# Kernel tuning notes

Measured on AMD Instinct MI355X. Metric: run time of the kernel, lower is better.

The kernel has to match this reference:

```python
import jax, jax.numpy as jnp
import numpy as np

B_, H_, W_, C_ = 8, 56, 56, 96
D_ = int(C_ * 2.0)          # d_inner = 192
N_ = 16                     # d_state
K_ = 4                      # scan directions
R_ = (C_ + 15) // 16        # dt_rank 'auto' = 6
MLP_H = 4 * C_
EPS = 1e-5


def setup_inputs() -> dict:
    key = jax.random.key(0)
    ks = jax.random.split(key, 16)
    s = 0.02
    rn = lambda k, sh, sc=1.0: jax.random.normal(k, sh, dtype=jnp.float32) * sc
    return dict(
        x=rn(ks[0], (B_, H_, W_, C_)),
        ln1_w=jnp.ones((C_,), jnp.float32), ln1_b=jnp.zeros((C_,), jnp.float32),
        in_proj_w=rn(ks[1], (2 * D_, C_), s),
        conv_w=rn(ks[2], (D_, 1, 3, 3), s), conv_b=jnp.zeros((D_,), jnp.float32),
        x_proj_w=rn(ks[3], (K_, R_ + 2 * N_, D_), s),
        dt_proj_w=rn(ks[4], (K_, D_, R_), s),
        dt_proj_b=rn(ks[5], (K_, D_), 0.1),
        A_logs=jax.random.uniform(ks[6], (K_ * D_, N_), jnp.float32, 0.0, 3.0),
        Ds=jnp.ones((K_ * D_,), jnp.float32),
        out_norm_w=jnp.ones((D_,), jnp.float32), out_norm_b=jnp.zeros((D_,), jnp.float32),
        out_proj_w=rn(ks[7], (C_, D_), s),
        ln2_w=jnp.ones((C_,), jnp.float32), ln2_b=jnp.zeros((C_,), jnp.float32),
        fc1_w=rn(ks[8], (MLP_H, C_), s), fc1_b=jnp.zeros((MLP_H,), jnp.float32),
        fc2_w=rn(ks[9], (C_, MLP_H), s), fc2_b=jnp.zeros((C_,), jnp.float32),
    )


def layer_norm(x, w, b):
    m = x.mean(-1, keepdims=True)
    v = ((x - m) ** 2).mean(-1, keepdims=True)
    return (x - m) / jnp.sqrt(v + EPS) * w + b


def ss2d(x, in_proj_w, conv_w, conv_b, x_proj_w, dt_proj_w, dt_proj_b,
         A_logs, Ds, out_norm_w, out_norm_b, out_proj_w):
    Bn, Hh, Ww, C = x.shape
    L = Hh * Ww
    xz = x @ in_proj_w.T                       # (B,H,W,2D)
    xc, z = jnp.split(xz, 2, axis=-1)
    xc = xc.transpose(0, 3, 1, 2)              # (B,D,H,W)
    xc = jax.lax.conv_general_dilated(xc, conv_w, (1, 1), 'SAME',
                                      feature_group_count=D_)
    xc = jax.nn.silu(xc + conv_b[None, :, None, None])
    # cross-scan: 4 traversal orders, each (B,D,L)
    x0 = xc.reshape(Bn, D_, L)
    x1 = xc.transpose(0, 1, 3, 2).reshape(Bn, D_, L)
    xs = jnp.stack([x0, x1, x0[..., ::-1], x1[..., ::-1]], axis=1)  # (B,K,D,L)
    xdbl = jnp.einsum('bkdl,kcd->bkcl', xs, x_proj_w)
    dts, Bs, Cs = jnp.split(xdbl, [R_, R_ + N_], axis=2)            # (B,K,R,L),(B,K,N,L)x2
    dts = jnp.einsum('bkrl,kdr->bkdl', dts, dt_proj_w)
    dts = jax.nn.softplus(dts + dt_proj_b[None, :, :, None])        # (B,K,D,L)
    A = -jnp.exp(A_logs).reshape(K_, D_, N_)                        # (K,D,N)

    def step(h, inp):
        xt, dtt, Bt, Ct = inp                  # (B,K,D),(B,K,D),(B,K,N),(B,K,N)
        h = h * jnp.exp(dtt[..., None] * A) + (dtt * xt)[..., None] * Bt[:, :, None, :]
        return h, jnp.einsum('bkdn,bkn->bkd', h, Ct)

    inps = (xs.transpose(3, 0, 1, 2), dts.transpose(3, 0, 1, 2),
            Bs.transpose(3, 0, 1, 2), Cs.transpose(3, 0, 1, 2))
    h0 = jnp.zeros((Bn, K_, D_, N_), jnp.float32)
    _, ys = jax.lax.scan(step, h0, inps)       # (L,B,K,D)
    ys = ys.transpose(1, 2, 3, 0)              # (B,K,D,L)
    ys = ys + Ds.reshape(K_, D_)[None, :, :, None] * xs
    # cross-merge: undo flips and transposed order
    y = ys[:, 0] + ys[:, 2, :, ::-1]
    y = y + (ys[:, 1] + ys[:, 3, :, ::-1]).reshape(Bn, D_, Ww, Hh) \
            .transpose(0, 1, 3, 2).reshape(Bn, D_, L)
    y = y.transpose(0, 2, 1).reshape(Bn, Hh, Ww, D_)
    y = layer_norm(y, out_norm_w, out_norm_b)
    y = y * jax.nn.silu(z)
    return y @ out_proj_w.T


def reference(x, ln1_w, ln1_b, in_proj_w, conv_w, conv_b, x_proj_w, dt_proj_w,
              dt_proj_b, A_logs, Ds, out_norm_w, out_norm_b, out_proj_w,
              ln2_w, ln2_b, fc1_w, fc1_b, fc2_w, fc2_b):
    # norm -> SS2D -> residual
    x = x + ss2d(layer_norm(x, ln1_w, ln1_b), in_proj_w, conv_w, conv_b,
                 x_proj_w, dt_proj_w, dt_proj_b, A_logs, Ds,
                 out_norm_w, out_norm_b, out_proj_w)
    # norm -> MLP -> residual
    h = layer_norm(x, ln2_w, ln2_b)
    h = jax.nn.gelu(h @ fc1_w.T + fc1_b) @ fc2_w.T + fc2_b
    return x + h
```

## Files before the change

kernel.cpp:

```cpp
#include <hip/hip_runtime.h>
#include <hip/hip_bf16.h>

typedef __hip_bfloat16 bf16;
typedef short bf16x8 __attribute__((ext_vector_type(8)));
typedef float f32x4 __attribute__((ext_vector_type(4)));

#define BBATCH 8
#define HHH 56
#define WWW 56
#define CCH 96
#define DIN 192
#define NST 16
#define KDIR 4
#define RDT 6
#define LLEN 3136
#define BLTOT 25088
#define SSEG 64
#define SEGL 49
#define PJC 38
#define PJW 152
#define PJS 40
#define PJS1 24
#define MLPH 384

#if defined(__has_builtin)
#if __has_builtin(__builtin_amdgcn_exp2f)
#define EXP2F(x) __builtin_amdgcn_exp2f(x)
#endif
#if __has_builtin(__builtin_amdgcn_logf)
#define LOG2F_(x) __builtin_amdgcn_logf(x)
#endif
#endif
#ifndef EXP2F
#define EXP2F(x) __expf((x) * 0.69314718056f)
#endif
#ifndef LOG2F_
#define LOG2F_(x) (__logf(x) * 1.44269504f)
#endif
#define LOG2E 1.44269504f

__device__ __forceinline__ float b2f(bf16 v) { return __bfloat162float(v); }
__device__ __forceinline__ bf16  f2b(float v) { return __float2bfloat16(v); }
__device__ __forceinline__ unsigned short f2bu(float f) {
    union { bf16 h; unsigned short u; } c; c.h = __float2bfloat16(f); return c.u;
}
__device__ __forceinline__ float sigm(float x) { return 1.f / (1.f + __expf(-x)); }
__device__ __forceinline__ float softplusf(float x) {
    float t = EXP2F(-fabsf(x) * LOG2E);
    return fmaxf(x, 0.f) + 0.69314718f * LOG2F_(1.f + t);
}
__device__ __forceinline__ float geluf(float v) {
    float u = 0.7978845608028654f * (v + 0.044715f * v * v * v);
    float ey = __expf(2.f * u);
    float th = 1.f - 2.f / (ey + 1.f);
    return 0.5f * v * (1.f + th);
}

__device__ __forceinline__ int pos_map(int k, int l) {
    if (k & 2) l = LLEN - 1 - l;
    if (k & 1) { int q = l / WWW; int r = l - q * WWW; return r * WWW + q; }
    return l;
}

__global__ __launch_bounds__(256) void ln_rows(
    const float* __restrict__ xin, const float* __restrict__ w,
    const float* __restrict__ b, unsigned short* __restrict__ xn) {
    int row = blockIdx.x * 4 + (threadIdx.x >> 6);
    int lane = threadIdx.x & 63;
    const float* xr = xin + (size_t)row * 96;
    float2 v = make_float2(0.f, 0.f);
    if (lane < 48) v = *(const float2*)&xr[lane * 2];
    float s = v.x + v.y, s2 = v.x * v.x + v.y * v.y;
    for (int o = 32; o; o >>= 1) {
        s += __shfl_down(s, o);
        s2 += __shfl_down(s2, o);
    }
    s = __shfl(s, 0); s2 = __shfl(s2, 0);
    float m = s * (1.f / 96.f);
    float var = s2 * (1.f / 96.f) - m * m;
    float rs = rsqrtf(var + 1e-5f);
    if (lane < 48) {
        float o0 = (v.x - m) * rs * w[lane * 2] + b[lane * 2];
        float o1 = (v.y - m) * rs * w[lane * 2 + 1] + b[lane * 2 + 1];
        ushort2 u; u.x = f2bu(o0); u.y = f2bu(o1);
        *(ushort2*)&xn[(size_t)row * 96 + lane * 2] = u;
    }
}

template<int N, int K, int EPI>
__global__ __launch_bounds__(256) void gemm_mfma(
    const unsigned short* __restrict__ X, const float* __restrict__ W,
    const float* __restrict__ bias, const float* __restrict__ res,
    void* __restrict__ out0v, void* __restrict__ out1v) {
    __shared__ unsigned short a_sh[256 * 40];
    __shared__ unsigned short b_sh[64 * 40];
    const int t = threadIdx.x;
    const int P0 = blockIdx.x * 256;
    const int N0 = blockIdx.y * 64;
    const int w = t >> 6, lane = t & 63, q = lane >> 4, nl = lane & 15;
    f32x4 acc[4][4];
#pragma unroll
    for (int i = 0; i < 4; ++i)
#pragma unroll
        for (int j = 0; j < 4; ++j)
            acc[i][j] = (f32x4){0.f, 0.f, 0.f, 0.f};
    for (int k0 = 0; k0 < K; k0 += 32) {
        __syncthreads();
#pragma unroll
        for (int it = 0; it < 4; ++it) {
            int idx = t + it * 256;
            int pr = idx >> 2, kq = idx & 3;
            uint4 v = *(const uint4*)&X[(size_t)(P0 + pr) * K + k0 + kq * 8];
            *(uint4*)&a_sh[pr * 40 + kq * 8] = v;
        }
#pragma unroll
        for (int it = 0; it < 2; ++it) {
            int idx = t + it * 256;
            int nr = idx >> 3, kq = idx & 7;
            int ng = N0 + nr; if (ng > N - 1) ng = N - 1;
            float4 v = *(const float4*)&W[(size_t)ng * K + k0 + kq * 4];
            ushort4 u;
            u.x = f2bu(v.x); u.y = f2bu(v.y); u.z = f2bu(v.z); u.w = f2bu(v.w);
            *(ushort4*)&b_sh[nr * 40 + kq * 4] = u;
        }
        __syncthreads();
        bf16x8 af[4], bfr[4];
#pragma unroll
        for (int mf = 0; mf < 4; ++mf)
            af[mf] = *(const bf16x8*)&a_sh[(w * 64 + mf * 16 + nl) * 40 + q * 8];
#pragma unroll
        for (int nf = 0; nf < 4; ++nf)
            bfr[nf] = *(const bf16x8*)&b_sh[(nf * 16 + nl) * 40 + q * 8];
#pragma unroll
        for (int mf = 0; mf < 4; ++mf)
#pragma unroll
            for (int nf = 0; nf < 4; ++nf)
                acc[mf][nf] = __builtin_amdgcn_mfma_f32_16x16x32_bf16(
                    af[mf], bfr[nf], acc[mf][nf], 0, 0, 0);
    }
#pragma unroll
    for (int mf = 0; mf < 4; ++mf) {
#pragma unroll
        for (int nf = 0; nf < 4; ++nf) {
#pragma unroll
            for (int r = 0; r < 4; ++r) {
                float v = acc[mf][nf][r];
                size_t pos = (size_t)P0 + w * 64 + mf * 16 + q * 4 + r;
                int n = N0 + nf * 16 + nl;
                if constexpr (EPI == 0) {
                    unsigned short* xc = (unsigned short*)out0v;
                    unsigned short* zz = (unsigned short*)out1v;
                    if (n < 192) xc[pos * 192 + n] = f2bu(v);
                    else         zz[pos * 192 + (n - 192)] = f2bu(v);
                } else if constexpr (EPI == 1) {
                    if (n < 152) ((float*)out0v)[pos * 152 + n] = v;
                } else if constexpr (EPI == 2) {
                    if (n < 96) ((float*)out0v)[pos * 96 + n] = res[pos * 96 + n] + v;
                } else if constexpr (EPI == 3) {
                    ((unsigned short*)out0v)[pos * 384 + n] = f2bu(geluf(v + bias[n]));
                } else {
                    if (n < 96) ((float*)out0v)[pos * 96 + n] =
                        res[pos * 96 + n] + bias[n] + v;
                }
            }
        }
    }
}

__global__ __launch_bounds__(256) void k2_conv(
    const unsigned short* __restrict__ xcpre, const float* __restrict__ cw,
    const float* __restrict__ cb, unsigned short* __restrict__ xconv) {
    int idx = blockIdx.x * 256 + threadIdx.x;
    int dd = idx % 96;
    int P = idx / 96;
    int d0 = dd * 2;
    int b = P / LLEN, l = P - b * LLEN;
    int h = l / WWW, w = l - h * WWW;
    float acc0 = cb[d0], acc1 = cb[d0 + 1];
#pragma unroll
    for (int i = 0; i < 3; ++i) {
        int hh = h + i - 1;
        if (hh < 0 || hh >= HHH) continue;
#pragma unroll
        for (int j = 0; j < 3; ++j) {
            int ww = w + j - 1;
            if (ww < 0 || ww >= WWW) continue;
            ushort2 xv = *(const ushort2*)&xcpre[
                ((size_t)(b * LLEN + hh * WWW + ww)) * DIN + d0];
            union { unsigned short u; bf16 h_; } c0, c1;
            c0.u = xv.x; c1.u = xv.y;
            acc0 = fmaf(b2f(c0.h_), cw[d0 * 9 + i * 3 + j], acc0);
            acc1 = fmaf(b2f(c1.h_), cw[(d0 + 1) * 9 + i * 3 + j], acc1);
        }
    }
    acc0 = acc0 * sigm(acc0);
    acc1 = acc1 * sigm(acc1);
    ushort2 o; o.x = f2bu(acc0); o.y = f2bu(acc1);
    *(ushort2*)&xconv[(size_t)P * DIN + d0] = o;
}

__global__ __launch_bounds__(192) void k4_scan1(
    const bf16* __restrict__ xconv, const float* __restrict__ proj,
    const float* __restrict__ dtw, const float* __restrict__ dtb,
    const float* __restrict__ Alog, float* __restrict__ hloc,
    float* __restrict__ tsum) {
    __shared__ float pl[SEGL * PJS1];
    __shared__ int posl[SEGL];
    const int bid = blockIdx.x;
    const int s = bid & 63, k = (bid >> 6) & 3, b = bid >> 8;
    const int d = threadIdx.x;
    const int l0 = s * SEGL;
    for (int q = d; q < SEGL * 22; q += 192) {
        int st = q / 22, c = q - st * 22;
        int p = pos_map(k, l0 + st);
        int ofs = (c < 6) ? c : c + 2;
        pl[st * PJS1 + ofs] = proj[(size_t)(b * LLEN + p) * PJW + k * PJC + c];
    }
    if (d < SEGL) posl[d] = pos_map(k, l0 + d) * DIN;
    float w6[RDT];
#pragma unroll
    for (int r = 0; r < RDT; ++r) w6[r] = dtw[(k * DIN + d) * RDT + r];
    const float bias = dtb[k * DIN + d];
    float a2[NST];
#pragma unroll
    for (int n = 0; n < NST; ++n)
        a2[n] = -__expf(Alog[(k * DIN + d) * NST + n]) * LOG2E;
    float h[NST];
#pragma unroll
    for (int n = 0; n < NST; ++n) h[n] = 0.f;
    float T = 0.f;
    __syncthreads();
    const bf16* xg = xconv + (size_t)b * LLEN * DIN + d;
    for (int bt = 0; bt < 7; ++bt) {
        int off7[7]; float xv7[7];
#pragma unroll
        for (int i = 0; i < 7; ++i) off7[i] = posl[bt * 7 + i];
#pragma unroll
        for (int i = 0; i < 7; ++i) xv7[i] = b2f(xg[off7[i]]);
#pragma unroll
        for (int i = 0; i < 7; ++i) {
            const float* rowf = &pl[(bt * 7 + i) * PJS1];
            float4 g0 = *(const float4*)(rowf);
            float2 g1 = *(const float2*)(rowf + 4);
            float dtv = bias;
            dtv = fmaf(g0.x, w6[0], dtv); dtv = fmaf(g0.y, w6[1], dtv);
            dtv = fmaf(g0.z, w6[2], dtv); dtv = fmaf(g0.w, w6[3], dtv);
            dtv = fmaf(g1.x, w6[4], dtv); dtv = fmaf(g1.y, w6[5], dtv);
            dtv = softplusf(dtv);
            T += dtv;
            float u = dtv * xv7[i];
#pragma unroll
            for (int g = 0; g < 4; ++g) {
                float4 Bv = *(const float4*)(rowf + 8 + 4 * g);
                float e0 = EXP2F(dtv * a2[4 * g + 0]);
                float e1 = EXP2F(dtv * a2[4 * g + 1]);
                float e2 = EXP2F(dtv * a2[4 * g + 2]);
                float e3 = EXP2F(dtv * a2[4 * g + 3]);
                h[4 * g + 0] = fmaf(h[4 * g + 0], e0, u * Bv.x);
                h[4 * g + 1] = fmaf(h[4 * g + 1], e1, u * Bv.y);
                h[4 * g + 2] = fmaf(h[4 * g + 2], e2, u * Bv.z);
                h[4 * g + 3] = fmaf(h[4 * g + 3], e3, u * Bv.w);
            }
        }
    }
    size_t base = ((size_t)bid * DIN + d) * NST;
#pragma unroll
    for (int n = 0; n < NST; ++n) hloc[base + n] = h[n];
    tsum[bid * DIN + d] = T;
}

__global__ __launch_bounds__(256) void k5_carry(
    const float* hloc, const float* __restrict__ tsum,
    const float* __restrict__ Alog, float* hin) {
    int g = blockIdx.x * 256 + threadIdx.x;
    int n = g & 15;
    int dk = g >> 4;
    int d = dk % DIN;
    int bk = dk / DIN;
    int k = bk & 3;
    float a2 = -__expf(Alog[(k * DIN + d) * NST + n]) * LOG2E;
    float Hc = 0.f;
    for (int s = 0; s < SSEG; ++s) {
        int bid = bk * SSEG + s;
        size_t idx = ((size_t)bid * DIN + d) * NST + n;
        float hl = hloc[idx];
        float Tv = tsum[bid * DIN + d];
        hin[idx] = Hc;
        Hc = fmaf(EXP2F(a2 * Tv), Hc, hl);
    }
}

__global__ __launch_bounds__(192) void k6_scan2(
    const bf16* __restrict__ xconv, const float* __restrict__ proj,
    const float* __restrict__ dtw, const float* __restrict__ dtb,
    const float* __restrict__ Alog, const float* __restrict__ Dsp,
    const float* __restrict__ hin, bf16* __restrict__ ysm) {
    __shared__ float pl[SEGL * PJS];
    __shared__ int posl[SEGL];
    const int bid = blockIdx.x;
    const int s = bid & 63, k = (bid >> 6) & 3, b = bid >> 8;
    const int d = threadIdx.x;
    const int l0 = s * SEGL;
    for (int q = d; q < SEGL * PJC; q += 192) {
        int st = q / PJC, c = q - st * PJC;
        int p = pos_map(k, l0 + st);
        int ofs = (c < 6) ? c : c + 2;
        pl[st * PJS + ofs] = proj[(size_t)(b * LLEN + p) * PJW + k * PJC + c];
    }
    if (d < SEGL) posl[d] = pos_map(k, l0 + d) * DIN;
    float w6[RDT];
#pragma unroll
    for (int r = 0; r < RDT; ++r) w6[r] = dtw[(k * DIN + d) * RDT + r];
    const float bias = dtb[k * DIN + d];
    const float dsv = Dsp[k * DIN + d];
    float a2[NST];
#pragma unroll
    for (int n = 0; n < NST; ++n)
        a2[n] = -__expf(Alog[(k * DIN + d) * NST + n]) * LOG2E;
    float h[NST];
    size_t hbase = ((size_t)bid * DIN + d) * NST;
#pragma unroll
    for (int n = 0; n < NST; ++n) h[n] = hin[hbase + n];
    __syncthreads();
    const bf16* xg = xconv + (size_t)b * LLEN * DIN + d;
    bf16* ysg = ysm + ((size_t)(b * KDIR + k) * LLEN) * DIN + d;
    for (int bt = 0; bt < 7; ++bt) {
        int off7[7]; float xv7[7];
#pragma unroll
        for (int i = 0; i < 7; ++i) off7[i] = posl[bt * 7 + i];
#pragma unroll
        for (int i = 0; i < 7; ++i) xv7[i] = b2f(xg[off7[i]]);
#pragma unroll
        for (int i = 0; i < 7; ++i) {
            const float* rowf = &pl[(bt * 7 + i) * PJS];
            float4 g0 = *(const float4*)(rowf);
            float2 g1 = *(const float2*)(rowf + 4);
            float dtv = bias;
            dtv = fmaf(g0.x, w6[0], dtv); dtv = fmaf(g0.y, w6[1], dtv);
            dtv = fmaf(g0.z, w6[2], dtv); dtv = fmaf(g0.w, w6[3], dtv);
            dtv = fmaf(g1.x, w6[4], dtv); dtv = fmaf(g1.y, w6[5], dtv);
            dtv = softplusf(dtv);
            float u = dtv * xv7[i];
            float y = dsv * xv7[i];
#pragma unroll
            for (int g = 0; g < 4; ++g) {
                float4 Bv = *(const float4*)(rowf + 8 + 4 * g);
                float4 Cv = *(const float4*)(rowf + 24 + 4 * g);
                float e0 = EXP2F(dtv * a2[4 * g + 0]);
                float e1 = EXP2F(dtv * a2[4 * g + 1]);
                float e2 = EXP2F(dtv * a2[4 * g + 2]);
                float e3 = EXP2F(dtv * a2[4 * g + 3]);
                h[4 * g + 0] = fmaf(h[4 * g + 0], e0, u * Bv.x);
                h[4 * g + 1] = fmaf(h[4 * g + 1], e1, u * Bv.y);
                h[4 * g + 2] = fmaf(h[4 * g + 2], e2, u * Bv.z);
                h[4 * g + 3] = fmaf(h[4 * g + 3], e3, u * Bv.w);
                y = fmaf(h[4 * g + 0], Cv.x, y);
                y = fmaf(h[4 * g + 1], Cv.y, y);
                y = fmaf(h[4 * g + 2], Cv.z, y);
                y = fmaf(h[4 * g + 3], Cv.w, y);
            }
            ysg[off7[i]] = f2b(y);
        }
    }
}

__global__ __launch_bounds__(256) void k65_merge(
    const bf16* __restrict__ ysm, const bf16* __restrict__ z,
    const float* __restrict__ onw, const float* __restrict__ onb,
    bf16* __restrict__ ymod) {
    __shared__ float rb[16 * DIN];
    __shared__ float ps[256], pq[256];
    __shared__ float mrow[16], srow[16];
    const int t = threadIdx.x;
    const int P0 = blockIdx.x * 16;
    for (int q = t; q < 16 * DIN; q += 256) {
        int pos = q / DIN, c = q - pos * DIN;
        int P = P0 + pos;
        int b = P / LLEN, l = P - b * LLEN;
        size_t base = ((size_t)(b * KDIR) * LLEN + l) * DIN + c;
        size_t pstr = (size_t)LLEN * DIN;
        float v = b2f(ysm[base]) + b2f(ysm[base + pstr]) +
                  b2f(ysm[base + 2 * pstr]) + b2f(ysm[base + 3 * pstr]);
        rb[q] = v;
    }
    __syncthreads();
    {
        int pos = t >> 4, part = t & 15;
        float s = 0.f, s2 = 0.f;
        for (int i = 0; i < 12; ++i) {
            float v = rb[pos * DIN + part * 12 + i];
            s += v; s2 += v * v;
        }
        ps[pos * 16 + part] = s; pq[pos * 16 + part] = s2;
    }
    __syncthreads();
    if (t < 16) {
        float s = 0.f, s2 = 0.f;
        for (int i = 0; i < 16; ++i) { s += ps[t * 16 + i]; s2 += pq[t * 16 + i]; }
        float m = s * (1.f / DIN);
        float v = s2 * (1.f / DIN) - m * m;
        mrow[t] = m; srow[t] = rsqrtf(v + 1e-5f);
    }
    __syncthreads();
    for (int q = t; q < 16 * DIN; q += 256) {
        int pos = q / DIN, c = q - pos * DIN;
        int P = P0 + pos;
        float v = (rb[q] - mrow[pos]) * srow[pos] * onw[c] + onb[c];
        float zv = b2f(z[(size_t)P * DIN + c]);
        v *= zv * sigm(zv);
        ymod[(size_t)P * DIN + c] = f2b(v);
    }
}

extern "C" void kernel_launch(void* const* d_in, const int* in_sizes, int n_in,
                              void* d_out, int out_size, void* d_ws, size_t ws_size,
                              hipStream_t stream) {
    const float* x      = (const float*)d_in[0];
    const float* ln1w   = (const float*)d_in[1];
    const float* ln1b   = (const float*)d_in[2];
    const float* inpW   = (const float*)d_in[3];
    const float* convW  = (const float*)d_in[4];
    const float* convB  = (const float*)d_in[5];
    const float* xprojW = (const float*)d_in[6];
    const float* dtW    = (const float*)d_in[7];
    const float* dtB    = (const float*)d_in[8];
    const float* Alog   = (const float*)d_in[9];
    const float* Dsp    = (const float*)d_in[10];
    const float* onw    = (const float*)d_in[11];
    const float* onb    = (const float*)d_in[12];
    const float* outW   = (const float*)d_in[13];
    const float* ln2w   = (const float*)d_in[14];
    const float* ln2b   = (const float*)d_in[15];
    const float* fc1W   = (const float*)d_in[16];
    const float* fc1b   = (const float*)d_in[17];
    const float* fc2W   = (const float*)d_in[18];
    const float* fc2b   = (const float*)d_in[19];
    float* out = (float*)d_out;

    char* ws = (char*)d_ws;
    unsigned short* z_us    = (unsigned short*)(ws + 0);
    bf16*  z_bf             = (bf16*)z_us;
    bf16*  xconv_bf         = (bf16*)(ws + 9633792);
    float* proj_f           = (float*)(ws + 19267584);
    bf16*  ymod_bf          = (bf16*)(ws + 19267584);
    unsigned short* xn_us   = (unsigned short*)(ws + 34521088);
    float* tsum_f           = (float*)(ws + 34521088);
    unsigned short* xcpre_us= (unsigned short*)(ws + 39337984);
    float* hloc_f           = (float*)(ws + 48971776);
    float* hin_f            = hloc_f;
    float* y1_f             = (float*)(ws + 48971776);
    unsigned short* y1n_us  = (unsigned short*)(ws + 58605568);
    bf16*  ysm_bf           = (bf16*)(ws + 74137600);
    unsigned short* hmlp_us = (unsigned short*)(ws + 74137600);

    ln_rows<<<6272, 256, 0, stream>>>(x, ln1w, ln1b, xn_us);
    gemm_mfma<384, 96, 0><<<dim3(98, 6), 256, 0, stream>>>(
        xn_us, inpW, nullptr, nullptr, xcpre_us, z_us);
    k2_conv<<<9408, 256, 0, stream>>>(xcpre_us, convW, convB,
                                      (unsigned short*)xconv_bf);
    gemm_mfma<152, 192, 1><<<dim3(98, 3), 256, 0, stream>>>(
        (const unsigned short*)xconv_bf, xprojW, nullptr, nullptr, proj_f, nullptr);
    k4_scan1<<<2048, 192, 0, stream>>>(xconv_bf, proj_f, dtW, dtB, Alog, hloc_f, tsum_f);
    k5_carry<<<384, 256, 0, stream>>>(hloc_f, tsum_f, Alog, hin_f);
    k6_scan2<<<2048, 192, 0, stream>>>(xconv_bf, proj_f, dtW, dtB, Alog, Dsp, hin_f, ysm_bf);
    k65_merge<<<1568, 256, 0, stream>>>(ysm_bf, z_bf, onw, onb, ymod_bf);
    gemm_mfma<96, 192, 2><<<dim3(98, 2), 256, 0, stream>>>(
        (const unsigned short*)ymod_bf, outW, nullptr, x, y1_f, nullptr);
    ln_rows<<<6272, 256, 0, stream>>>(y1_f, ln2w, ln2b, y1n_us);
    gemm_mfma<384, 96, 3><<<dim3(98, 6), 256, 0, stream>>>(
        y1n_us, fc1W, fc1b, nullptr, hmlp_us, nullptr);
    gemm_mfma<96, 384, 4><<<dim3(98, 2), 256, 0, stream>>>(
        hmlp_us, fc2W, fc2b, y1_f, out, nullptr);
}
```

Before: 396.6 us.

## Split scan state across thread pairs and halve GEMM row tiles

The two selective-scan kernels now give each (direction, channel) pair two threads. Each thread holds 8 of the 16 state entries, and the partial outputs are combined with a lane shuffle. The GEMM tile shrinks from 256 to 128 rows, which doubles the grid. The aim is more parallelism and occupancy on a GPU that was underfilled by 98-block GEMM grids and serial per-thread 16-state scans. In exchange, dt/softplus and the x loads are computed redundantly in both threads, a shuffle is added per step, and B-tile reuse per block drops.

```diff
diff --git a/kernel.cpp b/kernel.cpp
--- a/kernel.cpp
+++ b/kernel.cpp
@@ -92,22 +92,22 @@
     const unsigned short* __restrict__ X, const float* __restrict__ W,
     const float* __restrict__ bias, const float* __restrict__ res,
     void* __restrict__ out0v, void* __restrict__ out1v) {
-    __shared__ unsigned short a_sh[256 * 40];
+    __shared__ unsigned short a_sh[128 * 40];
     __shared__ unsigned short b_sh[64 * 40];
     const int t = threadIdx.x;
-    const int P0 = blockIdx.x * 256;
+    const int P0 = blockIdx.x * 128;
     const int N0 = blockIdx.y * 64;
     const int w = t >> 6, lane = t & 63, q = lane >> 4, nl = lane & 15;
-    f32x4 acc[4][4];
-#pragma unroll
-    for (int i = 0; i < 4; ++i)
+    f32x4 acc[2][4];
+#pragma unroll
+    for (int i = 0; i < 2; ++i)
 #pragma unroll
         for (int j = 0; j < 4; ++j)
             acc[i][j] = (f32x4){0.f, 0.f, 0.f, 0.f};
     for (int k0 = 0; k0 < K; k0 += 32) {
         __syncthreads();
 #pragma unroll
-        for (int it = 0; it < 4; ++it) {
+        for (int it = 0; it < 2; ++it) {
             int idx = t + it * 256;
             int pr = idx >> 2, kq = idx & 3;
             uint4 v = *(const uint4*)&X[(size_t)(P0 + pr) * K + k0 + kq * 8];
@@ -124,28 +124,28 @@
             *(ushort4*)&b_sh[nr * 40 + kq * 4] = u;
         }
         __syncthreads();
-        bf16x8 af[4], bfr[4];
-#pragma unroll
-        for (int mf = 0; mf < 4; ++mf)
-            af[mf] = *(const bf16x8*)&a_sh[(w * 64 + mf * 16 + nl) * 40 + q * 8];
+        bf16x8 af[2], bfr[4];
+#pragma unroll
+        for (int mf = 0; mf < 2; ++mf)
+            af[mf] = *(const bf16x8*)&a_sh[(w * 32 + mf * 16 + nl) * 40 + q * 8];
 #pragma unroll
         for (int nf = 0; nf < 4; ++nf)
             bfr[nf] = *(const bf16x8*)&b_sh[(nf * 16 + nl) * 40 + q * 8];
 #pragma unroll
-        for (int mf = 0; mf < 4; ++mf)
+        for (int mf = 0; mf < 2; ++mf)
 #pragma unroll
             for (int nf = 0; nf < 4; ++nf)
                 acc[mf][nf] = __builtin_amdgcn_mfma_f32_16x16x32_bf16(
                     af[mf], bfr[nf], acc[mf][nf], 0, 0, 0);
     }
 #pragma unroll
-    for (int mf = 0; mf < 4; ++mf) {
+    for (int mf = 0; mf < 2; ++mf) {
 #pragma unroll
         for (int nf = 0; nf < 4; ++nf) {
 #pragma unroll
             for (int r = 0; r < 4; ++r) {
                 float v = acc[mf][nf][r];
-                size_t pos = (size_t)P0 + w * 64 + mf * 16 + q * 4 + r;
+                size_t pos = (size_t)P0 + w * 32 + mf * 16 + q * 4 + r;
                 int n = N0 + nf * 16 + nl;
                 if constexpr (EPI == 0) {
                     unsigned short* xc = (unsigned short*)out0v;
@@ -199,7 +199,7 @@
     *(ushort2*)&xconv[(size_t)P * DIN + d0] = o;
 }
 
-__global__ __launch_bounds__(192) void k4_scan1(
+__global__ __launch_bounds__(384) void k4_scan1(
     const bf16* __restrict__ xconv, const float* __restrict__ proj,
     const float* __restrict__ dtw, const float* __restrict__ dtb,
     const float* __restrict__ Alog, float* __restrict__ hloc,
@@ -208,26 +208,27 @@
     __shared__ int posl[SEGL];
     const int bid = blockIdx.x;
     const int s = bid & 63, k = (bid >> 6) & 3, b = bid >> 8;
-    const int d = threadIdx.x;
+    const int t = threadIdx.x;
+    const int d = t >> 1, half = t & 1;
     const int l0 = s * SEGL;
-    for (int q = d; q < SEGL * 22; q += 192) {
+    for (int q = t; q < SEGL * 22; q += 384) {
         int st = q / 22, c = q - st * 22;
         int p = pos_map(k, l0 + st);
         int ofs = (c < 6) ? c : c + 2;
         pl[st * PJS1 + ofs] = proj[(size_t)(b * LLEN + p) * PJW + k * PJC + c];
     }
-    if (d < SEGL) posl[d] = pos_map(k, l0 + d) * DIN;
+    if (t < SEGL) posl[t] = pos_map(k, l0 + t) * DIN;
     float w6[RDT];
 #pragma unroll
     for (int r = 0; r < RDT; ++r) w6[r] = dtw[(k * DIN + d) * RDT + r];
     const float bias = dtb[k * DIN + d];
-    float a2[NST];
-#pragma unroll
-    for (int n = 0; n < NST; ++n)
-        a2[n] = -__expf(Alog[(k * DIN + d) * NST + n]) * LOG2E;
-    float h[NST];
-#pragma unroll
-    for (int n = 0; n < NST; ++n) h[n] = 0.f;
+    float a2[8];
+#pragma unroll
+    for (int j = 0; j < 8; ++j)
+        a2[j] = -__expf(Alog[(k * DIN + d) * NST + half * 8 + j]) * LOG2E;
+    float h[8];
+#pragma unroll
+    for (int j = 0; j < 8; ++j) h[j] = 0.f;
     float T = 0.f;
     __syncthreads();
     const bf16* xg = xconv + (size_t)b * LLEN * DIN + d;
@@ -249,24 +250,26 @@
             dtv = softplusf(dtv);
             T += dtv;
             float u = dtv * xv7[i];
-#pragma unroll
-            for (int g = 0; g < 4; ++g) {
-                float4 Bv = *(const float4*)(rowf + 8 + 4 * g);
-                float e0 = EXP2F(dtv * a2[4 * g + 0]);
-                float e1 = EXP2F(dtv * a2[4 * g + 1]);
-                float e2 = EXP2F(dtv * a2[4 * g + 2]);
-                float e3 = EXP2F(dtv * a2[4 * g + 3]);
-                h[4 * g + 0] = fmaf(h[4 * g + 0], e0, u * Bv.x);
-                h[4 * g + 1] = fmaf(h[4 * g + 1], e1, u * Bv.y);
-                h[4 * g + 2] = fmaf(h[4 * g + 2], e2, u * Bv.z);
-                h[4 * g + 3] = fmaf(h[4 * g + 3], e3, u * Bv.w);
+            float4 B0 = *(const float4*)(rowf + 8 + half * 8);
+            float4 B1 = *(const float4*)(rowf + 12 + half * 8);
+#pragma unroll
+            for (int j = 0; j < 4; ++j) {
+                float Bv = (j == 0) ? B0.x : (j == 1) ? B0.y : (j == 2) ? B0.z : B0.w;
+                float e = EXP2F(dtv * a2[j]);
+                h[j] = fmaf(h[j], e, u * Bv);
             }
-        }
-    }
-    size_t base = ((size_t)bid * DIN + d) * NST;
-#pragma unroll
-    for (int n = 0; n < NST; ++n) hloc[base + n] = h[n];
-    tsum[bid * DIN + d] = T;
+#pragma unroll
+            for (int j = 0; j < 4; ++j) {
+                float Bv = (j == 0) ? B1.x : (j == 1) ? B1.y : (j == 2) ? B1.z : B1.w;
+                float e = EXP2F(dtv * a2[4 + j]);
+                h[4 + j] = fmaf(h[4 + j], e, u * Bv);
+            }
+        }
+    }
+    size_t base = ((size_t)bid * DIN + d) * NST + half * 8;
+#pragma unroll
+    for (int j = 0; j < 8; ++j) hloc[base + j] = h[j];
+    if (half == 0) tsum[bid * DIN + d] = T;
 }
 
 __global__ __launch_bounds__(256) void k5_carry(
@@ -290,7 +293,7 @@
     }
 }
 
-__global__ __launch_bounds__(192) void k6_scan2(
+__global__ __launch_bounds__(384) void k6_scan2(
     const bf16* __restrict__ xconv, const float* __restrict__ proj,
     const float* __restrict__ dtw, const float* __restrict__ dtb,
     const float* __restrict__ Alog, const float* __restrict__ Dsp,
@@ -299,28 +302,29 @@
     __shared__ int posl[SEGL];
     const int bid = blockIdx.x;
     const int s = bid & 63, k = (bid >> 6) & 3, b = bid >> 8;
-    const int d = threadIdx.x;
+    const int t = threadIdx.x;
+    const int d = t >> 1, half = t & 1;
     const int l0 = s * SEGL;
-    for (int q = d; q < SEGL * PJC; q += 192) {
+    for (int q = t; q < SEGL * PJC; q += 384) {
         int st = q / PJC, c = q - st * PJC;
         int p = pos_map(k, l0 + st);
         int ofs = (c < 6) ? c : c + 2;
         pl[st * PJS + ofs] = proj[(size_t)(b * LLEN + p) * PJW + k * PJC + c];
     }
-    if (d < SEGL) posl[d] = pos_map(k, l0 + d) * DIN;
+    if (t < SEGL) posl[t] = pos_map(k, l0 + t) * DIN;
     float w6[RDT];
 #pragma unroll
     for (int r = 0; r < RDT; ++r) w6[r] = dtw[(k * DIN + d) * RDT + r];
     const float bias = dtb[k * DIN + d];
     const float dsv = Dsp[k * DIN + d];
-    float a2[NST];
-#pragma unroll
-    for (int n = 0; n < NST; ++n)
-        a2[n] = -__expf(Alog[(k * DIN + d) * NST + n]) * LOG2E;
-    float h[NST];
-    size_t hbase = ((size_t)bid * DIN + d) * NST;
-#pragma unroll
-    for (int n = 0; n < NST; ++n) h[n] = hin[hbase + n];
+    float a2[8];
+#pragma unroll
+    for (int j = 0; j < 8; ++j)
+        a2[j] = -__expf(Alog[(k * DIN + d) * NST + half * 8 + j]) * LOG2E;
+    float h[8];
+    size_t hbase = ((size_t)bid * DIN + d) * NST + half * 8;
+#pragma unroll
+    for (int j = 0; j < 8; ++j) h[j] = hin[hbase + j];
     __syncthreads();
     const bf16* xg = xconv + (size_t)b * LLEN * DIN + d;
     bf16* ysg = ysm + ((size_t)(b * KDIR + k) * LLEN) * DIN + d;
@@ -341,25 +345,29 @@
             dtv = fmaf(g1.x, w6[4], dtv); dtv = fmaf(g1.y, w6[5], dtv);
             dtv = softplusf(dtv);
             float u = dtv * xv7[i];
-            float y = dsv * xv7[i];
-#pragma unroll
-            for (int g = 0; g < 4; ++g) {
-                float4 Bv = *(const float4*)(rowf + 8 + 4 * g);
-                float4 Cv = *(const float4*)(rowf + 24 + 4 * g);
-                float e0 = EXP2F(dtv * a2[4 * g + 0]);
-                float e1 = EXP2F(dtv * a2[4 * g + 1]);
-                float e2 = EXP2F(dtv * a2[4 * g + 2]);
-                float e3 = EXP2F(dtv * a2[4 * g + 3]);
-                h[4 * g + 0] = fmaf(h[4 * g + 0], e0, u * Bv.x);
-                h[4 * g + 1] = fmaf(h[4 * g + 1], e1, u * Bv.y);
-                h[4 * g + 2] = fmaf(h[4 * g + 2], e2, u * Bv.z);
-                h[4 * g + 3] = fmaf(h[4 * g + 3], e3, u * Bv.w);
-                y = fmaf(h[4 * g + 0], Cv.x, y);
-                y = fmaf(h[4 * g + 1], Cv.y, y);
-                y = fmaf(h[4 * g + 2], Cv.z, y);
-                y = fmaf(h[4 * g + 3], Cv.w, y);
+            float y = 0.f;
+            float4 B0 = *(const float4*)(rowf + 8 + half * 8);
+            float4 B1 = *(const float4*)(rowf + 12 + half * 8);
+            float4 C0 = *(const float4*)(rowf + 24 + half * 8);
+            float4 C1 = *(const float4*)(rowf + 28 + half * 8);
+#pragma unroll
+            for (int j = 0; j < 4; ++j) {
+                float Bv = (j == 0) ? B0.x : (j == 1) ? B0.y : (j == 2) ? B0.z : B0.w;
+                float Cv = (j == 0) ? C0.x : (j == 1) ? C0.y : (j == 2) ? C0.z : C0.w;
+                float e = EXP2F(dtv * a2[j]);
+                h[j] = fmaf(h[j], e, u * Bv);
+                y = fmaf(h[j], Cv, y);
             }
-            ysg[off7[i]] = f2b(y);
+#pragma unroll
+            for (int j = 0; j < 4; ++j) {
+                float Bv = (j == 0) ? B1.x : (j == 1) ? B1.y : (j == 2) ? B1.z : B1.w;
+                float Cv = (j == 0) ? C1.x : (j == 1) ? C1.y : (j == 2) ? C1.z : C1.w;
+                float e = EXP2F(dtv * a2[4 + j]);
+                h[4 + j] = fmaf(h[4 + j], e, u * Bv);
+                y = fmaf(h[4 + j], Cv, y);
+            }
+            y += __shfl_xor(y, 1);
+            if (half == 0) ysg[off7[i]] = f2b(fmaf(dsv, xv7[i], y));
         }
     }
 }
@@ -454,21 +462,21 @@
     unsigned short* hmlp_us = (unsigned short*)(ws + 74137600);
 
     ln_rows<<<6272, 256, 0, stream>>>(x, ln1w, ln1b, xn_us);
-    gemm_mfma<384, 96, 0><<<dim3(98, 6), 256, 0, stream>>>(
+    gemm_mfma<384, 96, 0><<<dim3(196, 6), 256, 0, stream>>>(
         xn_us, inpW, nullptr, nullptr, xcpre_us, z_us);
     k2_conv<<<9408, 256, 0, stream>>>(xcpre_us, convW, convB,
                                       (unsigned short*)xconv_bf);
-    gemm_mfma<152, 192, 1><<<dim3(98, 3), 256, 0, stream>>>(
+    gemm_mfma<152, 192, 1><<<dim3(196, 3), 256, 0, stream>>>(
         (const unsigned short*)xconv_bf, xprojW, nullptr, nullptr, proj_f, nullptr);
-    k4_scan1<<<2048, 192, 0, stream>>>(xconv_bf, proj_f, dtW, dtB, Alog, hloc_f, tsum_f);
+    k4_scan1<<<2048, 384, 0, stream>>>(xconv_bf, proj_f, dtW, dtB, Alog, hloc_f, tsum_f);
     k5_carry<<<384, 256, 0, stream>>>(hloc_f, tsum_f, Alog, hin_f);
-    k6_scan2<<<2048, 192, 0, stream>>>(xconv_bf, proj_f, dtW, dtB, Alog, Dsp, hin_f, ysm_bf);
+    k6_scan2<<<2048, 384, 0, stream>>>(xconv_bf, proj_f, dtW, dtB, Alog, Dsp, hin_f, ysm_bf);
     k65_merge<<<1568, 256, 0, stream>>>(ysm_bf, z_bf, onw, onb, ymod_bf);
-    gemm_mfma<96, 192, 2><<<dim3(98, 2), 256, 0, stream>>>(
+    gemm_mfma<96, 192, 2><<<dim3(196, 2), 256, 0, stream>>>(
         (const unsigned short*)ymod_bf, outW, nullptr, x, y1_f, nullptr);
     ln_rows<<<6272, 256, 0, stream>>>(y1_f, ln2w, ln2b, y1n_us);
-    gemm_mfma<384, 96, 3><<<dim3(98, 6), 256, 0, stream>>>(
+    gemm_mfma<384, 96, 3><<<dim3(196, 6), 256, 0, stream>>>(
         y1n_us, fc1W, fc1b, nullptr, hmlp_us, nullptr);
-    gemm_mfma<96, 384, 4><<<dim3(98, 2), 256, 0, stream>>>(
+    gemm_mfma<96, 384, 4><<<dim3(196, 2), 256, 0, stream>>>(
         hmlp_us, fc2W, fc2b, y1_f, out, nullptr);
 }
```

Result: faster. 388.5 us (-2.0%).
